# Kernel tuning notes

Measured on AMD Instinct MI355X. Metric: run time of the kernel, lower is better.

The kernel has to match this reference:

```python
import jax, jax.numpy as jnp
import numpy as np

B, S, D, H = 4, 2048, 1024, 16
HD = D // H  # head_dim = 64


def rope(x):
    # canonical interleaved RoPE over the full feature dim, applied pre-head-split
    # x: [B, S, D]
    d = x.shape[-1]
    inv_freq = 1.0 / (10000.0 ** (jnp.arange(0, d, 2, dtype=jnp.float32) / d))  # [D/2]
    pos = jnp.arange(x.shape[1], dtype=jnp.float32)
    ang = pos[:, None] * inv_freq[None, :]          # [S, D/2]
    cos, sin = jnp.cos(ang), jnp.sin(ang)
    x1, x2 = x[..., 0::2], x[..., 1::2]             # even/odd pairs
    r1 = x1 * cos - x2 * sin
    r2 = x1 * sin + x2 * cos
    return jnp.stack([r1, r2], axis=-1).reshape(x.shape)


def setup_inputs() -> dict:
    key = jax.random.key(0)
    ks = jax.random.split(key, 9)
    s = 1.0 / np.sqrt(D)
    def lin(k):
        kw, kb = jax.random.split(k)
        W = jax.random.uniform(kw, (D, D), jnp.float32, -s, s)
        b = jax.random.uniform(kb, (D,), jnp.float32, -s, s)
        return W, b
    Wq, bq = lin(ks[0]); Wk, bk = lin(ks[1]); Wv, bv = lin(ks[2]); W0, b0 = lin(ks[3])
    x = jax.random.normal(ks[4], (B, S, D), jnp.float32)
    return {"x": x, "Wq": Wq, "bq": bq, "Wk": Wk, "bk": bk,
            "Wv": Wv, "bv": bv, "W0": W0, "b0": b0}


def reference(x, Wq, bq, Wk, bk, Wv, bv, W0, b0):
    # QKV projections (torch Linear: x @ W.T + b; here W stored as [in, out])
    q = x @ Wq + bq
    k = x @ Wk + bk
    v = x @ Wv + bv
    # RoPE applied to full d_model before head split (as in the source)
    q = rope(q)
    k = rope(k)
    # split heads -> [B, H, S, HD]
    b, s, _ = x.shape
    qh = q.reshape(b, s, H, HD).transpose(0, 2, 1, 3)
    kh = k.reshape(b, s, H, HD).transpose(0, 2, 1, 3)
    vh = v.reshape(b, s, H, HD).transpose(0, 2, 1, 3)
    scores = jnp.einsum("bhqd,bhkd->bhqk", qh, kh) / jnp.sqrt(jnp.float32(HD))
    attn = jax.nn.softmax(scores, axis=-1)  # dropout p=0.0 -> identity
    out = jnp.einsum("bhqk,bhkd->bhqd", attn, vh)
    out = out.transpose(0, 2, 1, 3).reshape(b, s, D)
    return out @ W0 + b0
```

## Files before the change

kernel.cpp:

```cpp
#include <hip/hip_runtime.h>
#include <hip/hip_bf16.h>

typedef unsigned short u16;
typedef u16 u16x8 __attribute__((ext_vector_type(8)));
typedef float f32x4 __attribute__((ext_vector_type(4)));
typedef __bf16 bf16x8 __attribute__((ext_vector_type(8)));

#define B_ 4
#define S_ 2048
#define D_ 1024
#define H_ 16
#define HD_ 64
#define M_ (B_*S_)

#if __has_builtin(__builtin_amdgcn_exp2f)
#define EXP2(x) __builtin_amdgcn_exp2f(x)
#else
#define EXP2(x) exp2f(x)
#endif

__device__ __forceinline__ f32x4 MFMA(u16x8 a, u16x8 b, f32x4 c) {
  return __builtin_amdgcn_mfma_f32_16x16x32_bf16(
      __builtin_bit_cast(bf16x8, a), __builtin_bit_cast(bf16x8, b), c, 0, 0, 0);
}

__device__ __forceinline__ u16 f2b(float f) {
  return __builtin_bit_cast(u16, __float2bfloat16(f));
}

__device__ __forceinline__ void load_lds16(const void* g, void* l) {
  __builtin_amdgcn_global_load_lds(
      (const __attribute__((address_space(1))) void*)g,
      (__attribute__((address_space(3))) void*)l, 16, 0, 0);
}

__device__ __forceinline__ unsigned int cvtpk(float lo, float hi) {
  unsigned int r;
  asm("v_cvt_pk_bf16_f32 %0, %1, %2" : "=v"(r) : "v"(lo), "v"(hi));
  return r;
}

__global__ __launch_bounds__(256) void k_rope_tab(float2* __restrict__ tab) {
  int i = blockIdx.x * 256 + threadIdx.x;
  if (i >= S_ * (D_ / 2)) return;
  int s = i >> 9;
  int f = i & 511;
  float invf = (float)exp(-(double)f / 512.0 * 9.210340371976184);
  float ang = (float)s * invf;
  tab[i] = make_float2(cosf(ang), sinf(ang));
}

__global__ __launch_bounds__(256) void k_cvt(const float* __restrict__ x,
                                             u16* __restrict__ xb, int n) {
  int i = blockIdx.x * 256 + threadIdx.x;
  if (i * 4 >= n) return;
  float4 v = ((const float4*)x)[i];
  ushort4 o;
  o.x = f2b(v.x); o.y = f2b(v.y); o.z = f2b(v.z); o.w = f2b(v.w);
  ((ushort4*)xb)[i] = o;
}

__global__ __launch_bounds__(256) void k_transpose4(
    const float* __restrict__ Wq, const float* __restrict__ Wk,
    const float* __restrict__ Wv, const float* __restrict__ W0,
    u16* __restrict__ Tq, u16* __restrict__ Tk, u16* __restrict__ Tv,
    u16* __restrict__ T0) {
  const float* W = (blockIdx.z == 0) ? Wq : (blockIdx.z == 1) ? Wk
                   : (blockIdx.z == 2) ? Wv : W0;
  u16* WT = (blockIdx.z == 0) ? Tq : (blockIdx.z == 1) ? Tk
            : (blockIdx.z == 2) ? Tv : T0;
  __shared__ float t[32][33];
  int tx = threadIdx.x, ty = threadIdx.y;
  int bx = blockIdx.x * 32, by = blockIdx.y * 32;
#pragma unroll
  for (int j = 0; j < 32; j += 8)
    t[ty + j][tx] = W[(size_t)(by + ty + j) * D_ + bx + tx];
  __syncthreads();
#pragma unroll
  for (int j = 0; j < 32; j += 8)
    WT[(size_t)(bx + ty + j) * D_ + by + tx] = f2b(t[tx][ty + j]);
}

template <int NM>
__global__ __launch_bounds__(512, 2) void k_gemm256(
    const u16* __restrict__ A, const u16* __restrict__ BT,
    const float* __restrict__ b0p, const float* __restrict__ b1p,
    const float* __restrict__ b2p, const float2* __restrict__ tab,
    u16* __restrict__ O0, u16* __restrict__ O1, u16* __restrict__ O2,
    float* __restrict__ FO) {
  __shared__ __attribute__((aligned(16))) u16 Al0[16384], Al1[16384];
  __shared__ __attribute__((aligned(16))) u16 Bl0[16384], Bl1[16384];
  const int tid = threadIdx.x;
  const int lane = tid & 63, wid = tid >> 6;
  const int wm = wid >> 2, wn = wid & 3;
  const int g = lane >> 4, c = lane & 15;
  const int flat = blockIdx.x;
  const int xcd = flat & 7, idx = flat >> 3;
  const int bx = xcd * 4 + (idx & 3), by = idx >> 2;
  const int rowbase = bx * 256;

  const int rr_ = tid >> 3, slot = tid & 7;
  const int sw8 = slot ^ (rr_ & 7);
  const u16* aB = A + (size_t)(rowbase + rr_) * 1024 + sw8 * 8;
  const u16* bB = BT + (size_t)(by * 256 + rr_) * 1024 + sw8 * 8;
  const int wdst = wid * 512;

  f32x4 acc[8][4] = {};
  const int swz = (c & 7) << 3;
  const int k0o = (g * 8) ^ swz;
  const int k1o = k0o ^ 32;
  const int ArdB = (wm * 128 + c) * 64;
  const int BrdB = (wn * 64 + c) * 64;

  u16x8 bf00, bf01, bf10, bf11, bf20, bf21, bf30, bf31;

#define ISSUE_LO(NA, NB, KT)                                                 \
  load_lds16(aB + (KT), &NA[wdst]);                                          \
  load_lds16(aB + 65536 + (KT), &NA[4096 + wdst]);                           \
  load_lds16(bB + (KT), &NB[wdst]);                                          \
  load_lds16(bB + 65536 + (KT), &NB[4096 + wdst]);
#define ISSUE_HI(NA, NB, KT)                                                 \
  load_lds16(aB + 131072 + (KT), &NA[8192 + wdst]);                          \
  load_lds16(aB + 196608 + (KT), &NA[12288 + wdst]);                         \
  load_lds16(bB + 131072 + (KT), &NB[8192 + wdst]);                          \
  load_lds16(bB + 196608 + (KT), &NB[12288 + wdst]);
#define PBAR                                                                 \
  __builtin_amdgcn_sched_barrier(0);                                         \
  __builtin_amdgcn_s_barrier();                                              \
  asm volatile("s_waitcnt lgkmcnt(0)" ::: "memory");                         \
  __builtin_amdgcn_sched_barrier(0);                                         \
  __builtin_amdgcn_s_setprio(1);
#define PEND                                                                 \
  __builtin_amdgcn_s_setprio(0);                                             \
  __builtin_amdgcn_sched_barrier(0);                                         \
  __builtin_amdgcn_s_barrier();
#define LDB8(CB)                                                             \
  bf00 = *(const u16x8*)&CB[BrdB + k0o];                                     \
  bf01 = *(const u16x8*)&CB[BrdB + k1o];                                     \
  bf10 = *(const u16x8*)&CB[BrdB + 1024 + k0o];                              \
  bf11 = *(const u16x8*)&CB[BrdB + 1024 + k1o];                              \
  bf20 = *(const u16x8*)&CB[BrdB + 2048 + k0o];                              \
  bf21 = *(const u16x8*)&CB[BrdB + 2048 + k1o];                              \
  bf30 = *(const u16x8*)&CB[BrdB + 3072 + k0o];                              \
  bf31 = *(const u16x8*)&CB[BrdB + 3072 + k1o];
#define LDA4(CA, MI0)                                                        \
  a00 = *(const u16x8*)&CA[ArdB + (MI0) * 1024 + k0o];                       \
  a01 = *(const u16x8*)&CA[ArdB + (MI0) * 1024 + k1o];                       \
  a10 = *(const u16x8*)&CA[ArdB + (MI0 + 1) * 1024 + k0o];                   \
  a11 = *(const u16x8*)&CA[ArdB + (MI0 + 1) * 1024 + k1o];
#define MFMA16(MI0)                                                          \
  acc[MI0][0] = MFMA(a00, bf00, acc[MI0][0]);                                \
  acc[MI0][0] = MFMA(a01, bf01, acc[MI0][0]);                                \
  acc[MI0][1] = MFMA(a00, bf10, acc[MI0][1]);                                \
  acc[MI0][1] = MFMA(a01, bf11, acc[MI0][1]);                                \
  acc[MI0][2] = MFMA(a00, bf20, acc[MI0][2]);                                \
  acc[MI0][2] = MFMA(a01, bf21, acc[MI0][2]);                                \
  acc[MI0][3] = MFMA(a00, bf30, acc[MI0][3]);                                \
  acc[MI0][3] = MFMA(a01, bf31, acc[MI0][3]);                                \
  acc[MI0 + 1][0] = MFMA(a10, bf00, acc[MI0 + 1][0]);                        \
  acc[MI0 + 1][0] = MFMA(a11, bf01, acc[MI0 + 1][0]);                        \
  acc[MI0 + 1][1] = MFMA(a10, bf10, acc[MI0 + 1][1]);                        \
  acc[MI0 + 1][1] = MFMA(a11, bf11, acc[MI0 + 1][1]);                        \
  acc[MI0 + 1][2] = MFMA(a10, bf20, acc[MI0 + 1][2]);                        \
  acc[MI0 + 1][2] = MFMA(a11, bf21, acc[MI0 + 1][2]);                        \
  acc[MI0 + 1][3] = MFMA(a10, bf30, acc[MI0 + 1][3]);                        \
  acc[MI0 + 1][3] = MFMA(a11, bf31, acc[MI0 + 1][3]);
#define TILE(CA, CB, NA, NB, KT, STG)                                        \
  {                                                                          \
    u16x8 a00, a01, a10, a11;                                                \
    if (STG) { ISSUE_LO(NA, NB, KT) }                                        \
    LDB8(CB) LDA4(CA, 0)                                                     \
    PBAR MFMA16(0) PEND                                                      \
    if (STG) { ISSUE_HI(NA, NB, KT) }                                        \
    LDA4(CA, 2) PBAR MFMA16(2) PEND                                          \
    LDA4(CA, 4) PBAR MFMA16(4) PEND                                          \
    LDA4(CA, 6) PBAR MFMA16(6)                                               \
    __builtin_amdgcn_s_setprio(0);                                           \
    __syncthreads();                                                         \
  }

  ISSUE_LO(Al0, Bl0, 0)
  ISSUE_HI(Al0, Bl0, 0)
  __syncthreads();

#pragma unroll 1
  for (int it = 0; it < 7; ++it) {
    const int kt1 = (2 * it + 1) * 64, kt2 = (2 * it + 2) * 64;
    TILE(Al0, Bl0, Al1, Bl1, kt1, 1)
    TILE(Al1, Bl1, Al0, Bl0, kt2, 1)
  }
  TILE(Al0, Bl0, Al1, Bl1, 15 * 64, 1)
  TILE(Al1, Bl1, Al0, Bl0, 0, 0)

  if (NM == 0) {
    const int mode = by >> 2;
    const float* bias = (mode == 0) ? b0p : (mode == 1) ? b1p : b2p;
    u16* Cout = (mode == 0) ? O0 : (mode == 1) ? O1 : O2;
    const int colL0 = (by & 3) * 256 + wn * 64;
    int coln[4];
    float bn[4];
#pragma unroll
    for (int ni = 0; ni < 4; ++ni) {
      coln[ni] = colL0 + ni * 16 + c;
      bn[ni] = bias[coln[ni]];
    }
    if (mode == 2) {
#pragma unroll
      for (int mi = 0; mi < 8; ++mi) {
        const int row0 = rowbase + wm * 128 + mi * 16 + g * 4;
        const int s0 = row0 & (S_ - 1);
        const int bidx = row0 >> 11;
#pragma unroll
        for (int ni = 0; ni < 4; ++ni) {
          const int h = coln[ni] >> 6, hd = coln[ni] & 63;
          ushort4 w;
          w.x = f2b(acc[mi][ni][0] + bn[ni]);
          w.y = f2b(acc[mi][ni][1] + bn[ni]);
          w.z = f2b(acc[mi][ni][2] + bn[ni]);
          w.w = f2b(acc[mi][ni][3] + bn[ni]);
          *(ushort4*)(Cout + ((size_t)(bidx * H_ + h) * HD_ + hd) * S_ + s0) = w;
        }
      }
    } else {
      const float qs = 0.18033688011112042f;
#pragma unroll
      for (int mi = 0; mi < 8; ++mi) {
#pragma unroll
        for (int rq = 0; rq < 4; ++rq) {
          const int row = rowbase + wm * 128 + mi * 16 + g * 4 + rq;
          const int s = row & (S_ - 1);
          const int bidx = row >> 11;
#pragma unroll
          for (int ni = 0; ni < 4; ++ni) {
            float v = acc[mi][ni][rq] + bn[ni];
            float2 cs = tab[(size_t)s * 512 + (coln[ni] >> 1)];
            float nb = __shfl_xor(v, 1);
            v = (lane & 1) ? (nb * cs.y + v * cs.x) : (v * cs.x - nb * cs.y);
            if (mode == 0) v *= qs;
            const int h = coln[ni] >> 6, hd = coln[ni] & 63;
            Cout[(((size_t)(bidx * H_ + h)) * S_ + s) * HD_ + hd] = f2b(v);
          }
        }
      }
    }
  } else {
    const int colb = by * 256 + wn * 64;
#pragma unroll
    for (int mi = 0; mi < 8; ++mi) {
#pragma unroll
      for (int rq = 0; rq < 4; ++rq) {
        const int row = rowbase + wm * 128 + mi * 16 + g * 4 + rq;
#pragma unroll
        for (int ni = 0; ni < 4; ++ni) {
          const int coln = colb + ni * 16 + c;
          FO[(size_t)row * D_ + coln] = acc[mi][ni][rq] + b0p[coln];
        }
      }
    }
  }
#undef TILE
#undef MFMA16
#undef LDA4
#undef LDB8
#undef PEND
#undef PBAR
#undef ISSUE_HI
#undef ISSUE_LO
}

__global__ __launch_bounds__(256, 4) void k_attn(const u16* __restrict__ Qh,
                                                 const u16* __restrict__ Kh,
                                                 const u16* __restrict__ Vt,
                                                 u16* __restrict__ AO) {
  __shared__ __attribute__((aligned(16))) u16 Kl0[4096], Kl1[4096];
  __shared__ __attribute__((aligned(16))) u16 Vl0[4096], Vl1[4096];
  __shared__ __attribute__((aligned(16))) u16 Pl[4096];
  const int tid = threadIdx.x;
  const int lane = tid & 63, wid = tid >> 6;
  const int g = lane >> 4, c = lane & 15;
  const int flat = blockIdx.y * 32 + blockIdx.x;
  const int swzid = (flat & 7) * 256 + (flat >> 3);
  const int qt = swzid & 31, bh = swzid >> 5;
  const size_t base = (size_t)bh * S_ * HD_;
  const int qr0 = qt * 64 + wid * 16;

  u16x8 qf[2];
#pragma unroll
  for (int ks = 0; ks < 2; ++ks)
    qf[ks] = *(const u16x8*)(Qh + base + (size_t)(qr0 + c) * HD_ + ks * 32 + g * 8);

  f32x4 o2[4] = {};
  float L = 0.f;

  const int swz = (c & 7) << 3;
  const int kb0 = c * 64 + ((g * 8) ^ swz);
  const int kb1 = c * 64 + ((32 + g * 8) ^ swz);
  const int pw0 = wid * 1024 + ((c * 64 + 0 * 16 + g * 4) ^ swz);
  const int pw1 = wid * 1024 + ((c * 64 + 1 * 16 + g * 4) ^ swz);
  const int pw2 = wid * 1024 + ((c * 64 + 2 * 16 + g * 4) ^ swz);
  const int pw3 = wid * 1024 + ((c * 64 + 3 * 16 + g * 4) ^ swz);
  const int pb0 = wid * 1024 + kb0;
  const int pb1 = wid * 1024 + kb1;
  const f32x4 z4 = {0.f, 0.f, 0.f, 0.f};

  const int ldrow = lane >> 3, ldslot = lane & 7;
  const int key0 = wid * 16 + ldrow, key1 = wid * 16 + 8 + ldrow;
  const u16* kp0 = Kh + base + (size_t)key0 * HD_ + (ldslot ^ (key0 & 7)) * 8;
  const u16* kp1 = Kh + base + (size_t)key1 * HD_ + (ldslot ^ (key1 & 7)) * 8;
  const u16* vp0 = Vt + base + (size_t)key0 * S_ + (ldslot ^ (key0 & 7)) * 8;
  const u16* vp1 = Vt + base + (size_t)key1 * S_ + (ldslot ^ (key1 & 7)) * 8;
  const int kdst0 = (wid * 16) * 64, kdst1 = (wid * 16 + 8) * 64;

#define STAGE(KP, VP)                                                        \
  {                                                                          \
    load_lds16(kp0, &KP[kdst0]); kp0 += 64 * HD_;                            \
    load_lds16(kp1, &KP[kdst1]); kp1 += 64 * HD_;                            \
    load_lds16(vp0, &VP[kdst0]); vp0 += 64;                                  \
    load_lds16(vp1, &VP[kdst1]); vp1 += 64;                                  \
  }

#define BODY(KC, VC, KP, VP)                                                 \
  {                                                                          \
    STAGE(KP, VP);                                                           \
    f32x4 s4[4];                                                             \
    __builtin_amdgcn_s_setprio(1);                                           \
    _Pragma("unroll") for (int n = 0; n < 4; ++n) {                          \
      u16x8 kfa = *(const u16x8*)&KC[n * 1024 + kb0];                        \
      u16x8 kfb = *(const u16x8*)&KC[n * 1024 + kb1];                        \
      s4[n] = MFMA(kfa, qf[0], z4);                                          \
      s4[n] = MFMA(kfb, qf[1], s4[n]);                                       \
    }                                                                        \
    __builtin_amdgcn_s_setprio(0);                                           \
    float p[4][4];                                                           \
    float rs = 0.f;                                                          \
    _Pragma("unroll") for (int n = 0; n < 4; ++n)                            \
        _Pragma("unroll") for (int r = 0; r < 4; ++r) {                      \
      p[n][r] = EXP2(s4[n][r]);                                              \
      rs += p[n][r];                                                         \
    }                                                                        \
    L += rs;                                                                 \
    {                                                                        \
      uint2 w0, w1, w2, w3;                                                  \
      w0.x = cvtpk(p[0][0], p[0][1]); w0.y = cvtpk(p[0][2], p[0][3]);        \
      w1.x = cvtpk(p[1][0], p[1][1]); w1.y = cvtpk(p[1][2], p[1][3]);        \
      w2.x = cvtpk(p[2][0], p[2][1]); w2.y = cvtpk(p[2][2], p[2][3]);        \
      w3.x = cvtpk(p[3][0], p[3][1]); w3.y = cvtpk(p[3][2], p[3][3]);        \
      *(uint2*)&Pl[pw0] = w0; *(uint2*)&Pl[pw1] = w1;                        \
      *(uint2*)&Pl[pw2] = w2; *(uint2*)&Pl[pw3] = w3;                        \
    }                                                                        \
    asm volatile("s_waitcnt lgkmcnt(0)" ::: "memory");                       \
    __builtin_amdgcn_sched_barrier(0);                                       \
    __builtin_amdgcn_s_setprio(1);                                           \
    {                                                                        \
      u16x8 pa0 = *(const u16x8*)&Pl[pb0];                                   \
      u16x8 pa1 = *(const u16x8*)&Pl[pb1];                                   \
      _Pragma("unroll") for (int nd = 0; nd < 4; ++nd) {                     \
        u16x8 va0 = *(const u16x8*)&VC[nd * 1024 + kb0];                     \
        u16x8 va1 = *(const u16x8*)&VC[nd * 1024 + kb1];                     \
        o2[nd] = MFMA(va0, pa0, o2[nd]);                                     \
        o2[nd] = MFMA(va1, pa1, o2[nd]);                                     \
      }                                                                      \
    }                                                                        \
    __builtin_amdgcn_s_setprio(0);                                           \
    __syncthreads();                                                         \
  }

  STAGE(Kl0, Vl0);
  __syncthreads();

#pragma unroll 1
  for (int it = 0; it < 16; ++it) {
    BODY(Kl0, Vl0, Kl1, Vl1);
    BODY(Kl1, Vl1, Kl0, Vl0);
  }

  L += __shfl_xor(L, 16);
  L += __shfl_xor(L, 32);
  const float inv = 1.f / L;
  const int b = bh >> 4, h = bh & (H_ - 1);
#pragma unroll
  for (int nd = 0; nd < 4; ++nd) {
    ushort4 w;
    w.x = f2b(o2[nd][0] * inv);
    w.y = f2b(o2[nd][1] * inv);
    w.z = f2b(o2[nd][2] * inv);
    w.w = f2b(o2[nd][3] * inv);
    *(ushort4*)(AO + ((size_t)(b * S_ + qr0 + c)) * D_ + h * HD_ + nd * 16 + g * 4) = w;
  }
#undef BODY
#undef STAGE
}

extern "C" void kernel_launch(void* const* d_in, const int* in_sizes, int n_in,
                              void* d_out, int out_size, void* d_ws,
                              size_t ws_size, hipStream_t stream) {
  const float* x  = (const float*)d_in[0];
  const float* Wq = (const float*)d_in[1];
  const float* bq = (const float*)d_in[2];
  const float* Wk = (const float*)d_in[3];
  const float* bk = (const float*)d_in[4];
  const float* Wv = (const float*)d_in[5];
  const float* bv = (const float*)d_in[6];
  const float* W0 = (const float*)d_in[7];
  const float* b0 = (const float*)d_in[8];
  float* out = (float*)d_out;

  char* ws = (char*)d_ws;
  const size_t MiB = (size_t)1 << 20;
  float2* tab = (float2*)(ws + 0);
  u16* xb  = (u16*)(ws + 8 * MiB);
  u16* WqT = (u16*)(ws + 24 * MiB);
  u16* WkT = (u16*)(ws + 26 * MiB);
  u16* WvT = (u16*)(ws + 28 * MiB);
  u16* W0T = (u16*)(ws + 30 * MiB);
  u16* Qh  = (u16*)(ws + 32 * MiB);
  u16* Kh  = (u16*)(ws + 48 * MiB);
  u16* Vt  = (u16*)(ws + 64 * MiB);
  u16* AO  = (u16*)(ws + 80 * MiB);

  k_rope_tab<<<4096, 256, 0, stream>>>(tab);
  k_cvt<<<(M_ * D_ / 4 + 255) / 256, 256, 0, stream>>>(x, xb, M_ * D_);
  k_transpose4<<<dim3(32, 32, 4), dim3(32, 8), 0, stream>>>(
      Wq, Wk, Wv, W0, WqT, WkT, WvT, W0T);
  k_gemm256<0><<<384, 512, 0, stream>>>(xb, WqT, bq, bk, bv, tab,
                                        Qh, Kh, Vt, nullptr);
  k_attn<<<dim3(S_ / 64, B_ * H_), 256, 0, stream>>>(Qh, Kh, Vt, AO);
  k_gemm256<1><<<128, 512, 0, stream>>>(AO, W0T, b0, nullptr, nullptr, nullptr,
                                        nullptr, nullptr, nullptr, out);
}
```

Before: 214.2 us.

## Enlarge attention query tile to 256 rows with 8 waves each handling 32 rows

The attention kernel now launches 512 blocks of 512 threads. Each block covers 256 query rows, and each wave computes two 16-row query groups that share the same K and V fragments read from LDS. The aim is to cut K/V global traffic and LDS fragment reads per query row. Each thread also issues half as many staging loads. The cost is a larger P buffer in LDS, twice the accumulator registers per thread, and fewer, larger blocks, which may reduce occupancy under the launch bound of 4.

```diff
diff --git a/kernel.cpp b/kernel.cpp
--- a/kernel.cpp
+++ b/kernel.cpp
@@ -268,97 +268,102 @@
 #undef ISSUE_LO
 }
 
-__global__ __launch_bounds__(256, 4) void k_attn(const u16* __restrict__ Qh,
+__global__ __launch_bounds__(512, 4) void k_attn(const u16* __restrict__ Qh,
                                                  const u16* __restrict__ Kh,
                                                  const u16* __restrict__ Vt,
                                                  u16* __restrict__ AO) {
   __shared__ __attribute__((aligned(16))) u16 Kl0[4096], Kl1[4096];
   __shared__ __attribute__((aligned(16))) u16 Vl0[4096], Vl1[4096];
-  __shared__ __attribute__((aligned(16))) u16 Pl[4096];
+  __shared__ __attribute__((aligned(16))) u16 Pl[16384];
   const int tid = threadIdx.x;
   const int lane = tid & 63, wid = tid >> 6;
   const int g = lane >> 4, c = lane & 15;
-  const int flat = blockIdx.y * 32 + blockIdx.x;
-  const int swzid = (flat & 7) * 256 + (flat >> 3);
-  const int qt = swzid & 31, bh = swzid >> 5;
+  const int flat = blockIdx.x;
+  const int swzid = (flat & 7) * 64 + (flat >> 3);
+  const int bh = swzid >> 3, qt = swzid & 7;
   const size_t base = (size_t)bh * S_ * HD_;
-  const int qr0 = qt * 64 + wid * 16;
-
-  u16x8 qf[2];
-#pragma unroll
-  for (int ks = 0; ks < 2; ++ks)
-    qf[ks] = *(const u16x8*)(Qh + base + (size_t)(qr0 + c) * HD_ + ks * 32 + g * 8);
-
-  f32x4 o2[4] = {};
-  float L = 0.f;
+  const int qr0 = qt * 256 + wid * 32;
+
+  u16x8 qf[2][2];
+#pragma unroll
+  for (int qg = 0; qg < 2; ++qg)
+#pragma unroll
+    for (int ks = 0; ks < 2; ++ks)
+      qf[qg][ks] = *(const u16x8*)(Qh + base +
+                                   (size_t)(qr0 + qg * 16 + c) * HD_ +
+                                   ks * 32 + g * 8);
+
+  f32x4 o20[4] = {}, o21[4] = {};
+  float L0 = 0.f, L1 = 0.f;
 
   const int swz = (c & 7) << 3;
   const int kb0 = c * 64 + ((g * 8) ^ swz);
   const int kb1 = c * 64 + ((32 + g * 8) ^ swz);
-  const int pw0 = wid * 1024 + ((c * 64 + 0 * 16 + g * 4) ^ swz);
-  const int pw1 = wid * 1024 + ((c * 64 + 1 * 16 + g * 4) ^ swz);
-  const int pw2 = wid * 1024 + ((c * 64 + 2 * 16 + g * 4) ^ swz);
-  const int pw3 = wid * 1024 + ((c * 64 + 3 * 16 + g * 4) ^ swz);
-  const int pb0 = wid * 1024 + kb0;
-  const int pb1 = wid * 1024 + kb1;
+  const int pwA0 = wid * 2048 + ((c * 64 + 0 * 16 + g * 4) ^ swz);
+  const int pwA1 = wid * 2048 + ((c * 64 + 1 * 16 + g * 4) ^ swz);
+  const int pwA2 = wid * 2048 + ((c * 64 + 2 * 16 + g * 4) ^ swz);
+  const int pwA3 = wid * 2048 + ((c * 64 + 3 * 16 + g * 4) ^ swz);
+  const int pbA0 = wid * 2048 + kb0;
+  const int pbA1 = wid * 2048 + kb1;
   const f32x4 z4 = {0.f, 0.f, 0.f, 0.f};
 
   const int ldrow = lane >> 3, ldslot = lane & 7;
-  const int key0 = wid * 16 + ldrow, key1 = wid * 16 + 8 + ldrow;
-  const u16* kp0 = Kh + base + (size_t)key0 * HD_ + (ldslot ^ (key0 & 7)) * 8;
-  const u16* kp1 = Kh + base + (size_t)key1 * HD_ + (ldslot ^ (key1 & 7)) * 8;
-  const u16* vp0 = Vt + base + (size_t)key0 * S_ + (ldslot ^ (key0 & 7)) * 8;
-  const u16* vp1 = Vt + base + (size_t)key1 * S_ + (ldslot ^ (key1 & 7)) * 8;
-  const int kdst0 = (wid * 16) * 64, kdst1 = (wid * 16 + 8) * 64;
+  const int srow = wid * 8 + ldrow;
+  const u16* kp0 = Kh + base + (size_t)srow * HD_ + (ldslot ^ (srow & 7)) * 8;
+  const u16* vp0 = Vt + base + (size_t)srow * S_ + (ldslot ^ (srow & 7)) * 8;
+  const int kdst0 = wid * 512;
 
 #define STAGE(KP, VP)                                                        \
   {                                                                          \
     load_lds16(kp0, &KP[kdst0]); kp0 += 64 * HD_;                            \
-    load_lds16(kp1, &KP[kdst1]); kp1 += 64 * HD_;                            \
     load_lds16(vp0, &VP[kdst0]); vp0 += 64;                                  \
-    load_lds16(vp1, &VP[kdst1]); vp1 += 64;                                  \
   }
 
 #define BODY(KC, VC, KP, VP)                                                 \
   {                                                                          \
     STAGE(KP, VP);                                                           \
-    f32x4 s4[4];                                                             \
+    f32x4 s40[4], s41[4];                                                    \
     __builtin_amdgcn_s_setprio(1);                                           \
     _Pragma("unroll") for (int n = 0; n < 4; ++n) {                          \
       u16x8 kfa = *(const u16x8*)&KC[n * 1024 + kb0];                        \
       u16x8 kfb = *(const u16x8*)&KC[n * 1024 + kb1];                        \
-      s4[n] = MFMA(kfa, qf[0], z4);                                          \
-      s4[n] = MFMA(kfb, qf[1], s4[n]);                                       \
+      s40[n] = MFMA(kfa, qf[0][0], z4);                                      \
+      s40[n] = MFMA(kfb, qf[0][1], s40[n]);                                  \
+      s41[n] = MFMA(kfa, qf[1][0], z4);                                      \
+      s41[n] = MFMA(kfb, qf[1][1], s41[n]);                                  \
     }                                                                        \
     __builtin_amdgcn_s_setprio(0);                                           \
-    float p[4][4];                                                           \
-    float rs = 0.f;                                                          \
-    _Pragma("unroll") for (int n = 0; n < 4; ++n)                            \
-        _Pragma("unroll") for (int r = 0; r < 4; ++r) {                      \
-      p[n][r] = EXP2(s4[n][r]);                                              \
-      rs += p[n][r];                                                         \
+    float rs0 = 0.f, rs1 = 0.f;                                              \
+    _Pragma("unroll") for (int n = 0; n < 4; ++n) {                          \
+      float p0[4], p1[4];                                                    \
+      _Pragma("unroll") for (int r = 0; r < 4; ++r) {                        \
+        p0[r] = EXP2(s40[n][r]); rs0 += p0[r];                               \
+        p1[r] = EXP2(s41[n][r]); rs1 += p1[r];                               \
+      }                                                                      \
+      uint2 w0, w1;                                                          \
+      w0.x = cvtpk(p0[0], p0[1]); w0.y = cvtpk(p0[2], p0[3]);                \
+      w1.x = cvtpk(p1[0], p1[1]); w1.y = cvtpk(p1[2], p1[3]);                \
+      const int pw = (n == 0) ? pwA0 : (n == 1) ? pwA1 : (n == 2) ? pwA2     \
+                                                                  : pwA3;   \
+      *(uint2*)&Pl[pw] = w0;                                                 \
+      *(uint2*)&Pl[pw + 1024] = w1;                                          \
     }                                                                        \
-    L += rs;                                                                 \
-    {                                                                        \
-      uint2 w0, w1, w2, w3;                                                  \
-      w0.x = cvtpk(p[0][0], p[0][1]); w0.y = cvtpk(p[0][2], p[0][3]);        \
-      w1.x = cvtpk(p[1][0], p[1][1]); w1.y = cvtpk(p[1][2], p[1][3]);        \
-      w2.x = cvtpk(p[2][0], p[2][1]); w2.y = cvtpk(p[2][2], p[2][3]);        \
-      w3.x = cvtpk(p[3][0], p[3][1]); w3.y = cvtpk(p[3][2], p[3][3]);        \
-      *(uint2*)&Pl[pw0] = w0; *(uint2*)&Pl[pw1] = w1;                        \
-      *(uint2*)&Pl[pw2] = w2; *(uint2*)&Pl[pw3] = w3;                        \
-    }                                                                        \
+    L0 += rs0; L1 += rs1;                                                    \
     asm volatile("s_waitcnt lgkmcnt(0)" ::: "memory");                       \
     __builtin_amdgcn_sched_barrier(0);                                       \
     __builtin_amdgcn_s_setprio(1);                                           \
     {                                                                        \
-      u16x8 pa0 = *(const u16x8*)&Pl[pb0];                                   \
-      u16x8 pa1 = *(const u16x8*)&Pl[pb1];                                   \
+      u16x8 pa00 = *(const u16x8*)&Pl[pbA0];                                 \
+      u16x8 pa01 = *(const u16x8*)&Pl[pbA1];                                 \
+      u16x8 pa10 = *(const u16x8*)&Pl[pbA0 + 1024];                          \
+      u16x8 pa11 = *(const u16x8*)&Pl[pbA1 + 1024];                          \
       _Pragma("unroll") for (int nd = 0; nd < 4; ++nd) {                     \
         u16x8 va0 = *(const u16x8*)&VC[nd * 1024 + kb0];                     \
         u16x8 va1 = *(const u16x8*)&VC[nd * 1024 + kb1];                     \
-        o2[nd] = MFMA(va0, pa0, o2[nd]);                                     \
-        o2[nd] = MFMA(va1, pa1, o2[nd]);                                     \
+        o20[nd] = MFMA(va0, pa00, o20[nd]);                                  \
+        o20[nd] = MFMA(va1, pa01, o20[nd]);                                  \
+        o21[nd] = MFMA(va0, pa10, o21[nd]);                                  \
+        o21[nd] = MFMA(va1, pa11, o21[nd]);                                  \
       }                                                                      \
     }                                                                        \
     __builtin_amdgcn_s_setprio(0);                                           \
@@ -374,18 +379,28 @@
     BODY(Kl1, Vl1, Kl0, Vl0);
   }
 
-  L += __shfl_xor(L, 16);
-  L += __shfl_xor(L, 32);
-  const float inv = 1.f / L;
+  L0 += __shfl_xor(L0, 16);
+  L0 += __shfl_xor(L0, 32);
+  L1 += __shfl_xor(L1, 16);
+  L1 += __shfl_xor(L1, 32);
+  const float inv0 = 1.f / L0, inv1 = 1.f / L1;
   const int b = bh >> 4, h = bh & (H_ - 1);
 #pragma unroll
   for (int nd = 0; nd < 4; ++nd) {
     ushort4 w;
-    w.x = f2b(o2[nd][0] * inv);
-    w.y = f2b(o2[nd][1] * inv);
-    w.z = f2b(o2[nd][2] * inv);
-    w.w = f2b(o2[nd][3] * inv);
-    *(ushort4*)(AO + ((size_t)(b * S_ + qr0 + c)) * D_ + h * HD_ + nd * 16 + g * 4) = w;
+    w.x = f2b(o20[nd][0] * inv0);
+    w.y = f2b(o20[nd][1] * inv0);
+    w.z = f2b(o20[nd][2] * inv0);
+    w.w = f2b(o20[nd][3] * inv0);
+    *(ushort4*)(AO + ((size_t)(b * S_ + qr0 + c)) * D_ + h * HD_ + nd * 16 +
+                g * 4) = w;
+    ushort4 w2;
+    w2.x = f2b(o21[nd][0] * inv1);
+    w2.y = f2b(o21[nd][1] * inv1);
+    w2.z = f2b(o21[nd][2] * inv1);
+    w2.w = f2b(o21[nd][3] * inv1);
+    *(ushort4*)(AO + ((size_t)(b * S_ + qr0 + 16 + c)) * D_ + h * HD_ +
+                nd * 16 + g * 4) = w2;
   }
 #undef BODY
 #undef STAGE
@@ -424,7 +439,7 @@
       Wq, Wk, Wv, W0, WqT, WkT, WvT, W0T);
   k_gemm256<0><<<384, 512, 0, stream>>>(xb, WqT, bq, bk, bv, tab,
                                         Qh, Kh, Vt, nullptr);
-  k_attn<<<dim3(S_ / 64, B_ * H_), 256, 0, stream>>>(Qh, Kh, Vt, AO);
+  k_attn<<<512, 512, 0, stream>>>(Qh, Kh, Vt, AO);
   k_gemm256<1><<<128, 512, 0, stream>>>(AO, W0T, b0, nullptr, nullptr, nullptr,
                                         nullptr, nullptr, nullptr, out);
 }
```

Measured after the change: 193.8 us. 1.11x faster.
